# Performance work log

Measured on AMD Instinct MI355X. Metric: run time of the kernel, lower is better.

## Reference

```python
import jax, jax.numpy as jnp
import numpy as np

EPS = 1e-6

def _rotate(z, q):
    # rotation trick (Householder-style reflection chain), z,q: [M, D]
    sg = jax.lax.stop_gradient
    z_norm = z / (jnp.linalg.norm(z, axis=1, keepdims=True) + EPS)
    q_norm = q / (jnp.linalg.norm(q, axis=1, keepdims=True) + EPS)
    w = sg((z_norm + q_norm) / jnp.linalg.norm(z_norm + q_norm, axis=1, keepdims=True))
    zn_d = sg(z_norm)
    qn_d = sg(q_norm)
    e = z - 2.0 * jnp.sum(z * w, axis=1, keepdims=True) * w \
          + 2.0 * jnp.sum(z * zn_d, axis=1, keepdims=True) * qn_d
    scale = sg(jnp.linalg.norm(q, axis=1, keepdims=True) / (jnp.linalg.norm(z, axis=1, keepdims=True) + EPS))
    return e * scale

def setup_inputs() -> dict:
    key = jax.random.key(0)
    k1, k2 = jax.random.split(key)
    x = jax.random.normal(k1, (16, 2048, 512), dtype=jnp.float32)
    codebooks = jax.random.normal(k2, (8, 1024, 512), dtype=jnp.float32)
    return {"x": x, "codebooks": codebooks}

def reference(x, codebooks):
    # x: [B, N, D]; codebooks: [Q, C, D]
    B, N, D = x.shape
    Q, C, _ = codebooks.shape
    sg = jax.lax.stop_gradient
    cb_sq = jnp.sum(codebooks * codebooks, axis=-1)  # [Q, C]
    residual = x
    quantized_out = jnp.zeros_like(x)
    all_indices = []
    all_losses = []
    for qi in range(Q):
        cb = codebooks[qi]                               # [C, D]
        flat = residual.reshape(-1, D)                   # [B*N, D]
        # squared euclidean distance: ||r||^2 - 2 r.c + ||c||^2
        d2 = jnp.sum(flat * flat, axis=1, keepdims=True) - 2.0 * (flat @ cb.T) + cb_sq[qi]
        ind = jnp.argmin(d2, axis=1)                     # [B*N]
        quant_raw = jnp.take(cb, ind, axis=0)            # [B*N, D]
        # commitment loss (codebook frozen per freeze_codebook=True)
        loss = jnp.mean((sg(quant_raw) - flat) ** 2)
        # rotation-trick transform of the quantized vectors
        quant = _rotate(flat, quant_raw).reshape(B, N, D)
        residual = residual - sg(quant)
        quantized_out = quantized_out + quant
        all_indices.append(ind.reshape(B, N))
        all_losses.append(loss)
    all_indices = jnp.stack(all_indices, axis=-1)        # [B, N, Q]
    all_losses = jnp.stack(all_losses, axis=-1)          # [Q]
    return quantized_out, all_indices, all_losses
```

## Files before the change

### kernel.cpp

```cpp
#include <hip/hip_runtime.h>

#define EPS 1e-6f

typedef __attribute__((ext_vector_type(8))) short bf16x8;
typedef __attribute__((ext_vector_type(4))) float f32x4;
typedef __attribute__((ext_vector_type(8))) unsigned short ushort8;

#define AS1(p) ((const __attribute__((address_space(1))) void*)(p))
#define AS3(p) ((__attribute__((address_space(3))) void*)(p))

__device__ inline unsigned int fkey(float f) {
  unsigned int u = __float_as_uint(f);
  return (u & 0x80000000u) ? ~u : (u | 0x80000000u);
}
__device__ inline float inv_fkey(unsigned int k) {
  unsigned int u = (k & 0x80000000u) ? (k & 0x7fffffffu) : ~k;
  return __uint_as_float(u);
}

__device__ inline unsigned long long shfl_xor_u64(unsigned long long v, int mask) {
  unsigned int lo = (unsigned int)(v & 0xffffffffull);
  unsigned int hi = (unsigned int)(v >> 32);
  lo = (unsigned int)__shfl_xor((int)lo, mask);
  hi = (unsigned int)__shfl_xor((int)hi, mask);
  return (((unsigned long long)hi) << 32) | lo;
}

__device__ inline unsigned short f2bf(float f) {
  unsigned int u = __float_as_uint(f);
  u += 0x7fffu + ((u >> 16) & 1u);
  return (unsigned short)(u >> 16);
}
__device__ inline float bf2f(unsigned short h) {
  return __uint_as_float(((unsigned int)h) << 16);
}

__device__ inline unsigned lds_off(const void* p) {
  return (unsigned)(unsigned long long)(__attribute__((address_space(3))) const void*)p;
}

template<int OFF>
__device__ inline bf16x8 ds_read128(unsigned addr) {
  bf16x8 r;
  asm volatile("ds_read_b128 %0, %1 offset:%2" : "=v"(r) : "v"(addr), "i"(OFF));
  return r;
}

template<int OFF>
__device__ inline float gload_f32(unsigned long long a) {
  float r;
  asm volatile("global_load_dword %0, %1, off offset:%2" : "=v"(r) : "v"(a), "i"(OFF));
  return r;
}

__global__ __launch_bounds__(256) void prep_kernel(
    const float* __restrict__ x, const float* __restrict__ cbs,
    unsigned short* __restrict__ Rhi, unsigned short* __restrict__ Rlo,
    unsigned short* __restrict__ CBhi, unsigned short* __restrict__ CBlo,
    float* __restrict__ cbsq, float* __restrict__ loss_out) {
  constexpr size_t M = 32768, D = 512, C = 1024, Q = 8;
  const size_t nthreads = (size_t)gridDim.x * 256;
  const size_t gtid = (size_t)blockIdx.x * 256 + threadIdx.x;
  const int lane = threadIdx.x & 63;
  const int w = threadIdx.x >> 6;

  for (size_t i = gtid; i < M * D / 8; i += nthreads) {
    size_t off = i * 8;
    float4 v0 = *(const float4*)(x + off);
    float4 v1 = *(const float4*)(x + off + 4);
    float v[8] = {v0.x, v0.y, v0.z, v0.w, v1.x, v1.y, v1.z, v1.w};
    ushort8 h, l;
    #pragma unroll
    for (int j = 0; j < 8; j++) {
      unsigned short hh = f2bf(v[j]);
      h[j] = hh;
      l[j] = f2bf(v[j] - bf2f(hh));
    }
    *(ushort8*)(Rhi + off) = h;
    *(ushort8*)(Rlo + off) = l;
  }
  for (size_t i = gtid; i < Q * C * D / 8; i += nthreads) {
    size_t off = i * 8;
    float4 v0 = *(const float4*)(cbs + off);
    float4 v1 = *(const float4*)(cbs + off + 4);
    float v[8] = {v0.x, v0.y, v0.z, v0.w, v1.x, v1.y, v1.z, v1.w};
    ushort8 h, l;
    #pragma unroll
    for (int j = 0; j < 8; j++) {
      unsigned short hh = f2bf(v[j]);
      h[j] = hh;
      l[j] = f2bf(v[j] - bf2f(hh));
    }
    *(ushort8*)(CBhi + off) = h;
    *(ushort8*)(CBlo + off) = l;
  }
  for (int row = blockIdx.x * 4 + w; row < (int)(Q * C); row += gridDim.x * 4) {
    const float4* p = (const float4*)(cbs + (size_t)row * 512);
    float4 v0 = p[lane];
    float4 v1 = p[lane + 64];
    float s = v0.x*v0.x + v0.y*v0.y + v0.z*v0.z + v0.w*v0.w
            + v1.x*v1.x + v1.y*v1.y + v1.z*v1.z + v1.w*v1.w;
    #pragma unroll
    for (int off = 32; off; off >>= 1) s += __shfl_xor(s, off);
    if (lane == 0) cbsq[row] = s;
  }
  if (blockIdx.x == 0 && threadIdx.x < (int)Q) loss_out[threadIdx.x] = 0.f;
}

#define BARRIER  asm volatile("s_barrier" ::: "memory")
#define LGKM0    asm volatile("s_waitcnt lgkmcnt(0)" ::: "memory")
#define SCHEDB   __builtin_amdgcn_sched_barrier(0)

__global__ __launch_bounds__(512, 2) void stage_kernel(
    const float* __restrict__ x, const float* __restrict__ cbs,
    unsigned short* __restrict__ Rhi, unsigned short* __restrict__ Rlo,
    const unsigned short* __restrict__ CBhi, const unsigned short* __restrict__ CBlo,
    const float* __restrict__ cbsq, float* __restrict__ qout,
    float* __restrict__ idx_out, float* __restrict__ loss_out) {
  __shared__ unsigned short As[3][2][128 * 32];
  __shared__ unsigned short Bs[3][2][256 * 32];
  __shared__ unsigned long long bestLDS[4][128];
  __shared__ float ls[8];

  const int tid = threadIdx.x;
  const int lane = tid & 63;
  const int w = tid >> 6;
  const int wr = w >> 2, wc = w & 3;
  const int row0 = blockIdx.x * 128;

  const int rw = lane >> 2, oq = lane & 3;
  const int o_sw = (oq - rw - (rw >> 2)) & 3;
  const int m = lane & 15, g = lane >> 4;
  const int f_sw8 = ((g + m + (m >> 2)) & 3) * 8;

  const unsigned short* pAhi = Rhi + (size_t)(row0 + w * 16 + rw) * 512 + o_sw * 8;
  const unsigned short* pAlo = Rlo + (size_t)(row0 + w * 16 + rw) * 512 + o_sw * 8;

  for (int qi = 0; qi < 8; ++qi) {
    const int last = (qi == 7);
    const size_t cbo = (size_t)qi * 524288;
    const unsigned short* pBhi = CBhi + cbo + (size_t)(w * 32 + rw) * 512 + o_sw * 8;
    const unsigned short* pBlo = CBlo + cbo + (size_t)(w * 32 + rw) * 512 + o_sw * 8;
    const float* cq_base = cbsq + (qi << 10);
    const float* cbq_f32 = cbs + cbo;

    unsigned aA = lds_off(&As[0][0][(wr * 64 + m) * 32 + f_sw8]);
    unsigned aB = lds_off(&Bs[0][0][(wc * 64 + m) * 32 + f_sw8]);

    unsigned long long best[4][4];
    #pragma unroll
    for (int mi = 0; mi < 4; mi++)
      #pragma unroll
      for (int r = 0; r < 4; r++) best[mi][r] = ~0ull;

    auto stageA = [&](int buf, int t) {
      const size_t ko = (size_t)((t & 15) * 32);
      __builtin_amdgcn_global_load_lds(AS1(pAhi + ko), AS3(&As[buf][0][w * 512]), 16, 0, 0);
      __builtin_amdgcn_global_load_lds(AS1(pAlo + ko), AS3(&As[buf][1][w * 512]), 16, 0, 0);
    };
    auto stageB1 = [&](int buf, int t) {
      const size_t ko = (size_t)((t & 15) * 32);
      const size_t cof = (size_t)((t >> 4) * 256) * 512;
      unsigned short* dBh = &Bs[buf][0][w * 1024];
      __builtin_amdgcn_global_load_lds(AS1(pBhi + cof + ko), AS3(dBh), 16, 0, 0);
      __builtin_amdgcn_global_load_lds(AS1(pBhi + cof + ko + 8192), AS3(dBh + 512), 16, 0, 0);
    };
    auto stageB2 = [&](int buf, int t) {
      const size_t ko = (size_t)((t & 15) * 32);
      const size_t cof = (size_t)((t >> 4) * 256) * 512;
      unsigned short* dBl = &Bs[buf][1][w * 1024];
      __builtin_amdgcn_global_load_lds(AS1(pBlo + cof + ko), AS3(dBl), 16, 0, 0);
      __builtin_amdgcn_global_load_lds(AS1(pBlo + cof + ko + 8192), AS3(dBl + 512), 16, 0, 0);
    };

    __syncthreads();

    float cq[4][4];
    {
      unsigned long long cqp = (unsigned long long)(cq_base + wc * 64 + m);
      cq[0][0] = gload_f32<0>(cqp);    cq[0][1] = gload_f32<64>(cqp);
      cq[0][2] = gload_f32<128>(cqp);  cq[0][3] = gload_f32<192>(cqp);
      cq[1][0] = gload_f32<1024>(cqp); cq[1][1] = gload_f32<1088>(cqp);
      cq[1][2] = gload_f32<1152>(cqp); cq[1][3] = gload_f32<1216>(cqp);
      cq[2][0] = gload_f32<2048>(cqp); cq[2][1] = gload_f32<2112>(cqp);
      cq[2][2] = gload_f32<2176>(cqp); cq[2][3] = gload_f32<2240>(cqp);
      cq[3][0] = gload_f32<3072>(cqp); cq[3][1] = gload_f32<3136>(cqp);
      cq[3][2] = gload_f32<3200>(cqp); cq[3][3] = gload_f32<3264>(cqp);
      asm volatile("s_waitcnt vmcnt(0)" ::: "memory");
    }

    stageA(0, 0); stageB1(0, 0); stageB2(0, 0);
    stageA(1, 1); stageB1(1, 1); stageB2(1, 1);
    asm volatile("s_waitcnt vmcnt(6)" ::: "memory");
    BARRIER;
    SCHEDB;

    bf16x8 ah[4], al[4], bh[4], bl[4];
    f32x4 acc[4][4];
    int bn = 0;
    int bst = 2;

    for (int t = 0; t < 64; ++t) {
      const int kk = t & 15;

      ah[0] = ds_read128<0>(aA);     ah[1] = ds_read128<1024>(aA);
      al[0] = ds_read128<8192>(aA);  al[1] = ds_read128<9216>(aA);
      bh[0] = ds_read128<0>(aB);     bh[1] = ds_read128<1024>(aB);
      bl[0] = ds_read128<16384>(aB); bl[1] = ds_read128<17408>(aB);
      if (t < 62) stageA(bst, t + 2);
      if (kk == 0) {
        #pragma unroll
        for (int mi = 0; mi < 4; mi++)
          #pragma unroll
          for (int ni = 0; ni < 4; ni++)
            acc[mi][ni] = (f32x4){0.f, 0.f, 0.f, 0.f};
      }
      BARRIER; LGKM0; SCHEDB;
      __builtin_amdgcn_s_setprio(1);
      #pragma unroll
      for (int mi = 0; mi < 2; mi++)
        #pragma unroll
        for (int ni = 0; ni < 2; ni++)
          acc[mi][ni] = __builtin_amdgcn_mfma_f32_16x16x32_bf16(ah[mi], bh[ni], acc[mi][ni], 0, 0, 0);
      #pragma unroll
      for (int mi = 0; mi < 2; mi++)
        #pragma unroll
        for (int ni = 0; ni < 2; ni++)
          acc[mi][ni] = __builtin_amdgcn_mfma_f32_16x16x32_bf16(ah[mi], bl[ni], acc[mi][ni], 0, 0, 0);
      #pragma unroll
      for (int mi = 0; mi < 2; mi++)
        #pragma unroll
        for (int ni = 0; ni < 2; ni++)
          acc[mi][ni] = __builtin_amdgcn_mfma_f32_16x16x32_bf16(al[mi], bh[ni], acc[mi][ni], 0, 0, 0);
      __builtin_amdgcn_s_setprio(0);
      BARRIER; SCHEDB;

      bh[2] = ds_read128<2048>(aB);  bh[3] = ds_read128<3072>(aB);
      bl[2] = ds_read128<18432>(aB); bl[3] = ds_read128<19456>(aB);
      if (t < 62) stageB1(bst, t + 2);
      BARRIER; LGKM0; SCHEDB;
      __builtin_amdgcn_s_setprio(1);
      #pragma unroll
      for (int mi = 0; mi < 2; mi++)
        #pragma unroll
        for (int ni = 2; ni < 4; ni++)
          acc[mi][ni] = __builtin_amdgcn_mfma_f32_16x16x32_bf16(ah[mi], bh[ni], acc[mi][ni], 0, 0, 0);
      #pragma unroll
      for (int mi = 0; mi < 2; mi++)
        #pragma unroll
        for (int ni = 2; ni < 4; ni++)
          acc[mi][ni] = __builtin_amdgcn_mfma_f32_16x16x32_bf16(ah[mi], bl[ni], acc[mi][ni], 0, 0, 0);
      #pragma unroll
      for (int mi = 0; mi < 2; mi++)
        #pragma unroll
        for (int ni = 2; ni < 4; ni++)
          acc[mi][ni] = __builtin_amdgcn_mfma_f32_16x16x32_bf16(al[mi], bh[ni], acc[mi][ni], 0, 0, 0);
      __builtin_amdgcn_s_setprio(0);
      BARRIER; SCHEDB;

      ah[2] = ds_read128<2048>(aA);  ah[3] = ds_read128<3072>(aA);
      al[2] = ds_read128<10240>(aA); al[3] = ds_read128<11264>(aA);
      if (t < 62) stageB2(bst, t + 2);
      BARRIER; LGKM0; SCHEDB;
      __builtin_amdgcn_s_setprio(1);
      #pragma unroll
      for (int mi = 2; mi < 4; mi++)
        #pragma unroll
        for (int ni = 2; ni < 4; ni++)
          acc[mi][ni] = __builtin_amdgcn_mfma_f32_16x16x32_bf16(ah[mi], bh[ni], acc[mi][ni], 0, 0, 0);
      #pragma unroll
      for (int mi = 2; mi < 4; mi++)
        #pragma unroll
        for (int ni = 2; ni < 4; ni++)
          acc[mi][ni] = __builtin_amdgcn_mfma_f32_16x16x32_bf16(ah[mi], bl[ni], acc[mi][ni], 0, 0, 0);
      #pragma unroll
      for (int mi = 2; mi < 4; mi++)
        #pragma unroll
        for (int ni = 2; ni < 4; ni++)
          acc[mi][ni] = __builtin_amdgcn_mfma_f32_16x16x32_bf16(al[mi], bh[ni], acc[mi][ni], 0, 0, 0);
      __builtin_amdgcn_s_setprio(0);
      BARRIER; SCHEDB;

      __builtin_amdgcn_s_setprio(1);
      #pragma unroll
      for (int mi = 2; mi < 4; mi++)
        #pragma unroll
        for (int ni = 0; ni < 2; ni++)
          acc[mi][ni] = __builtin_amdgcn_mfma_f32_16x16x32_bf16(ah[mi], bh[ni], acc[mi][ni], 0, 0, 0);
      #pragma unroll
      for (int mi = 2; mi < 4; mi++)
        #pragma unroll
        for (int ni = 0; ni < 2; ni++)
          acc[mi][ni] = __builtin_amdgcn_mfma_f32_16x16x32_bf16(ah[mi], bl[ni], acc[mi][ni], 0, 0, 0);
      #pragma unroll
      for (int mi = 2; mi < 4; mi++)
        #pragma unroll
        for (int ni = 0; ni < 2; ni++)
          acc[mi][ni] = __builtin_amdgcn_mfma_f32_16x16x32_bf16(al[mi], bh[ni], acc[mi][ni], 0, 0, 0);
      __builtin_amdgcn_s_setprio(0);
      if (kk == 15) {
        const int ct_ = t >> 4;
        const unsigned colb = ct_ * 256 + wc * 64 + m;
        #pragma unroll
        for (int mi = 0; mi < 4; mi++)
          #pragma unroll
          for (int r = 0; r < 4; r++) {
            #pragma unroll
            for (int ni = 0; ni < 4; ni++) {
              float d2 = fmaf(-2.f, acc[mi][ni][r], cq[ct_][ni]);
              unsigned long long p =
                  (((unsigned long long)fkey(d2)) << 32) | (colb + ni * 16);
              if (p < best[mi][r]) best[mi][r] = p;
            }
          }
      }
      if (t < 62) asm volatile("s_waitcnt vmcnt(6)" ::: "memory");
      else        asm volatile("s_waitcnt vmcnt(0)" ::: "memory");
      BARRIER; SCHEDB;

      const int s_ = (bn == 2) ? -2 : 1;
      aA += s_ * 16384; aB += s_ * 32768;
      bn = (bn == 2) ? 0 : bn + 1;
      bst = (bst == 2) ? 0 : bst + 1;
    }

    #pragma unroll
    for (int mi = 0; mi < 4; mi++)
      #pragma unroll
      for (int r = 0; r < 4; r++) {
        unsigned long long mn = best[mi][r];
        #pragma unroll
        for (int off = 1; off < 16; off <<= 1) {
          unsigned long long o = shfl_xor_u64(mn, off);
          if (o < mn) mn = o;
        }
        best[mi][r] = mn;
      }

    if (m == 0) {
      #pragma unroll
      for (int mi = 0; mi < 4; mi++)
        #pragma unroll
        for (int r = 0; r < 4; r++)
          bestLDS[wc][wr * 64 + mi * 16 + g * 4 + r] = best[mi][r];
    }
    __syncthreads();

    float lossacc = 0.f;
    #pragma unroll 2
    for (int rr = 0; rr < 16; rr++) {
      const int row128 = w * 16 + rr;
      unsigned long long mn = bestLDS[0][row128];
      #pragma unroll
      for (int q2 = 1; q2 < 4; q2++) {
        unsigned long long o = bestLDS[q2][row128];
        if (o < mn) mn = o;
      }
      const int c = (int)(mn & 0xffffffffu);
      const int row = row0 + row128;
      if (lane == 0) idx_out[(size_t)row * 8 + qi] = (float)c;

      const float qq = cq_base[c];
      const float d2b = inv_fkey((unsigned)(mn >> 32));
      const float zq = (qq - d2b) * 0.5f;

      const size_t base = (size_t)row * 512 + lane * 8;
      ushort8 h = *(const ushort8*)(Rhi + base);
      ushort8 l = *(const ushort8*)(Rlo + base);
      const float* qrow = cbq_f32 + (size_t)c * 512 + lane * 8;
      float4 q0 = *(const float4*)qrow;
      float4 q1 = *(const float4*)(qrow + 4);
      float z[8], q[8] = {q0.x, q0.y, q0.z, q0.w, q1.x, q1.y, q1.z, q1.w};
      #pragma unroll
      for (int j = 0; j < 8; j++) z[j] = bf2f(h[j]) + bf2f(l[j]);

      float zz = 0.f;
      #pragma unroll
      for (int j = 0; j < 8; j++) zz = fmaf(z[j], z[j], zz);
      #pragma unroll
      for (int off = 32; off; off >>= 1) zz += __shfl_xor(zz, off);

      float nz = sqrtf(zz), nq = sqrtf(qq);
      float inz = 1.f / (nz + EPS), inq = 1.f / (nq + EPS);
      float ns  = sqrtf(zz*inz*inz + 2.f*zq*inz*inq + qq*inq*inq);
      float ins = 1.f / ns;
      float zw  = (zz*inz + zq*inq) * ins;
      float zzn = zz * inz;
      float scale = nq * inz;
      float az = scale * (1.f - 2.f * zw * ins * inz);
      float aq = scale * (2.f * zzn - 2.f * zw * ins) * inq;

      if (!last) {
        #pragma unroll
        for (int j = 0; j < 8; j++) {
          float r = z[j] - (az * z[j] + aq * q[j]);
          unsigned short hh = f2bf(r);
          h[j] = hh;
          l[j] = f2bf(r - bf2f(hh));
        }
        *(ushort8*)(Rhi + base) = h;
        *(ushort8*)(Rlo + base) = l;
      } else {
        float4 x0 = *(const float4*)(x + base);
        float4 x1 = *(const float4*)(x + base + 4);
        float xv[8] = {x0.x, x0.y, x0.z, x0.w, x1.x, x1.y, x1.z, x1.w};
        float o[8];
        #pragma unroll
        for (int j = 0; j < 8; j++) {
          float r = z[j] - (az * z[j] + aq * q[j]);
          o[j] = xv[j] - r;
        }
        *(float4*)(qout + base)     = (float4){o[0], o[1], o[2], o[3]};
        *(float4*)(qout + base + 4) = (float4){o[4], o[5], o[6], o[7]};
      }
      lossacc += (zz - 2.f * zq + qq);
    }
    if (lane == 0) ls[w] = lossacc;
    __syncthreads();
    if (tid == 0)
      atomicAdd(loss_out + qi, (ls[0] + ls[1] + ls[2] + ls[3] +
                                ls[4] + ls[5] + ls[6] + ls[7]) *
                               (1.f / (32768.f * 512.f)));
  }
}

extern "C" void kernel_launch(void* const* d_in, const int* in_sizes, int n_in,
                              void* d_out, int out_size, void* d_ws, size_t ws_size,
                              hipStream_t stream) {
  const float* x   = (const float*)d_in[0];
  const float* cbs = (const float*)d_in[1];
  float* out = (float*)d_out;
  const size_t M = 32768, D = 512, Q = 8, C = 1024;
  float* qout     = out;
  float* idx_out  = out + M * D;
  float* loss_out = idx_out + M * Q;

  unsigned short* Rhi  = (unsigned short*)d_ws;
  unsigned short* Rlo  = Rhi + M * D;
  unsigned short* CBhi = Rlo + M * D;
  unsigned short* CBlo = CBhi + Q * C * D;
  float* cbsq = (float*)(CBlo + Q * C * D);

  prep_kernel<<<512, 256, 0, stream>>>(x, cbs, Rhi, Rlo, CBhi, CBlo, cbsq, loss_out);

  stage_kernel<<<256, 512, 0, stream>>>(
      x, cbs, Rhi, Rlo, CBhi, CBlo, cbsq, qout, idx_out, loss_out);
}
```

Baseline: 1.089 ms.

## Software-pipeline LDS fragment reads across K iterations with register double buffering

Restructures the bf16-split GEMM main loop so the A/B fragments for the next K step are read from LDS during the current step's MFMA phases, using double-buffered register arrays and a two-step unrolled loop. Full lgkmcnt(0) waits become partial lgkmcnt(4) waits, and the global vmcnt wait moves earlier into the second phase, so LDS latency overlaps with MFMA work. This raises register pressure (extra fragment buffers) under launch_bounds(512,2) and makes barrier and wait-count correctness more delicate.

```diff
diff --git a/kernel.cpp b/kernel.cpp
--- a/kernel.cpp
+++ b/kernel.cpp
@@ -108,8 +108,10 @@
 }
 
 #define BARRIER  asm volatile("s_barrier" ::: "memory")
-#define LGKM0    asm volatile("s_waitcnt lgkmcnt(0)" ::: "memory")
 #define SCHEDB   __builtin_amdgcn_sched_barrier(0)
+#define LGKM(N)  asm volatile("s_waitcnt lgkmcnt(" #N ")" ::: "memory")
+#define VMC(N)   asm volatile("s_waitcnt vmcnt(" #N ")" ::: "memory")
+#define MFMA1(d, a, b) d = __builtin_amdgcn_mfma_f32_16x16x32_bf16(a, b, d, 0, 0, 0)
 
 __global__ __launch_bounds__(512, 2) void stage_kernel(
     const float* __restrict__ x, const float* __restrict__ cbs,
@@ -186,143 +188,132 @@
       cq[2][2] = gload_f32<2176>(cqp); cq[2][3] = gload_f32<2240>(cqp);
       cq[3][0] = gload_f32<3072>(cqp); cq[3][1] = gload_f32<3136>(cqp);
       cq[3][2] = gload_f32<3200>(cqp); cq[3][3] = gload_f32<3264>(cqp);
-      asm volatile("s_waitcnt vmcnt(0)" ::: "memory");
-    }
-
-    stageA(0, 0); stageB1(0, 0); stageB2(0, 0);
-    stageA(1, 1); stageB1(1, 1); stageB2(1, 1);
-    asm volatile("s_waitcnt vmcnt(6)" ::: "memory");
-    BARRIER;
-    SCHEDB;
-
-    bf16x8 ah[4], al[4], bh[4], bl[4];
+      VMC(0);
+    }
+
+    bf16x8 A01h[2][2], A01l[2][2], B01h[2][2], B01l[2][2];
+    bf16x8 A23h[2], A23l[2], B23h[2], B23l[2];
     f32x4 acc[4][4];
     int bn = 0;
     int bst = 2;
 
-    for (int t = 0; t < 64; ++t) {
-      const int kk = t & 15;
-
-      ah[0] = ds_read128<0>(aA);     ah[1] = ds_read128<1024>(aA);
-      al[0] = ds_read128<8192>(aA);  al[1] = ds_read128<9216>(aA);
-      bh[0] = ds_read128<0>(aB);     bh[1] = ds_read128<1024>(aB);
-      bl[0] = ds_read128<16384>(aB); bl[1] = ds_read128<17408>(aB);
-      if (t < 62) stageA(bst, t + 2);
-      if (kk == 0) {
-        #pragma unroll
-        for (int mi = 0; mi < 4; mi++)
-          #pragma unroll
-          for (int ni = 0; ni < 4; ni++)
-            acc[mi][ni] = (f32x4){0.f, 0.f, 0.f, 0.f};
-      }
-      BARRIER; LGKM0; SCHEDB;
-      __builtin_amdgcn_s_setprio(1);
-      #pragma unroll
-      for (int mi = 0; mi < 2; mi++)
-        #pragma unroll
-        for (int ni = 0; ni < 2; ni++)
-          acc[mi][ni] = __builtin_amdgcn_mfma_f32_16x16x32_bf16(ah[mi], bh[ni], acc[mi][ni], 0, 0, 0);
-      #pragma unroll
-      for (int mi = 0; mi < 2; mi++)
-        #pragma unroll
-        for (int ni = 0; ni < 2; ni++)
-          acc[mi][ni] = __builtin_amdgcn_mfma_f32_16x16x32_bf16(ah[mi], bl[ni], acc[mi][ni], 0, 0, 0);
-      #pragma unroll
-      for (int mi = 0; mi < 2; mi++)
-        #pragma unroll
-        for (int ni = 0; ni < 2; ni++)
-          acc[mi][ni] = __builtin_amdgcn_mfma_f32_16x16x32_bf16(al[mi], bh[ni], acc[mi][ni], 0, 0, 0);
-      __builtin_amdgcn_s_setprio(0);
-      BARRIER; SCHEDB;
-
-      bh[2] = ds_read128<2048>(aB);  bh[3] = ds_read128<3072>(aB);
-      bl[2] = ds_read128<18432>(aB); bl[3] = ds_read128<19456>(aB);
-      if (t < 62) stageB1(bst, t + 2);
-      BARRIER; LGKM0; SCHEDB;
-      __builtin_amdgcn_s_setprio(1);
-      #pragma unroll
-      for (int mi = 0; mi < 2; mi++)
-        #pragma unroll
-        for (int ni = 2; ni < 4; ni++)
-          acc[mi][ni] = __builtin_amdgcn_mfma_f32_16x16x32_bf16(ah[mi], bh[ni], acc[mi][ni], 0, 0, 0);
-      #pragma unroll
-      for (int mi = 0; mi < 2; mi++)
-        #pragma unroll
-        for (int ni = 2; ni < 4; ni++)
-          acc[mi][ni] = __builtin_amdgcn_mfma_f32_16x16x32_bf16(ah[mi], bl[ni], acc[mi][ni], 0, 0, 0);
-      #pragma unroll
-      for (int mi = 0; mi < 2; mi++)
-        #pragma unroll
-        for (int ni = 2; ni < 4; ni++)
-          acc[mi][ni] = __builtin_amdgcn_mfma_f32_16x16x32_bf16(al[mi], bh[ni], acc[mi][ni], 0, 0, 0);
-      __builtin_amdgcn_s_setprio(0);
-      BARRIER; SCHEDB;
-
-      ah[2] = ds_read128<2048>(aA);  ah[3] = ds_read128<3072>(aA);
-      al[2] = ds_read128<10240>(aA); al[3] = ds_read128<11264>(aA);
-      if (t < 62) stageB2(bst, t + 2);
-      BARRIER; LGKM0; SCHEDB;
-      __builtin_amdgcn_s_setprio(1);
-      #pragma unroll
-      for (int mi = 2; mi < 4; mi++)
-        #pragma unroll
-        for (int ni = 2; ni < 4; ni++)
-          acc[mi][ni] = __builtin_amdgcn_mfma_f32_16x16x32_bf16(ah[mi], bh[ni], acc[mi][ni], 0, 0, 0);
-      #pragma unroll
-      for (int mi = 2; mi < 4; mi++)
-        #pragma unroll
-        for (int ni = 2; ni < 4; ni++)
-          acc[mi][ni] = __builtin_amdgcn_mfma_f32_16x16x32_bf16(ah[mi], bl[ni], acc[mi][ni], 0, 0, 0);
-      #pragma unroll
-      for (int mi = 2; mi < 4; mi++)
-        #pragma unroll
-        for (int ni = 2; ni < 4; ni++)
-          acc[mi][ni] = __builtin_amdgcn_mfma_f32_16x16x32_bf16(al[mi], bh[ni], acc[mi][ni], 0, 0, 0);
-      __builtin_amdgcn_s_setprio(0);
-      BARRIER; SCHEDB;
-
-      __builtin_amdgcn_s_setprio(1);
-      #pragma unroll
-      for (int mi = 2; mi < 4; mi++)
-        #pragma unroll
-        for (int ni = 0; ni < 2; ni++)
-          acc[mi][ni] = __builtin_amdgcn_mfma_f32_16x16x32_bf16(ah[mi], bh[ni], acc[mi][ni], 0, 0, 0);
-      #pragma unroll
-      for (int mi = 2; mi < 4; mi++)
-        #pragma unroll
-        for (int ni = 0; ni < 2; ni++)
-          acc[mi][ni] = __builtin_amdgcn_mfma_f32_16x16x32_bf16(ah[mi], bl[ni], acc[mi][ni], 0, 0, 0);
-      #pragma unroll
-      for (int mi = 2; mi < 4; mi++)
-        #pragma unroll
-        for (int ni = 0; ni < 2; ni++)
-          acc[mi][ni] = __builtin_amdgcn_mfma_f32_16x16x32_bf16(al[mi], bh[ni], acc[mi][ni], 0, 0, 0);
-      __builtin_amdgcn_s_setprio(0);
-      if (kk == 15) {
-        const int ct_ = t >> 4;
-        const unsigned colb = ct_ * 256 + wc * 64 + m;
-        #pragma unroll
-        for (int mi = 0; mi < 4; mi++)
-          #pragma unroll
-          for (int r = 0; r < 4; r++) {
-            #pragma unroll
-            for (int ni = 0; ni < 4; ni++) {
-              float d2 = fmaf(-2.f, acc[mi][ni][r], cq[ct_][ni]);
-              unsigned long long p =
-                  (((unsigned long long)fkey(d2)) << 32) | (colb + ni * 16);
-              if (p < best[mi][r]) best[mi][r] = p;
-            }
-          }
-      }
-      if (t < 62) asm volatile("s_waitcnt vmcnt(6)" ::: "memory");
-      else        asm volatile("s_waitcnt vmcnt(0)" ::: "memory");
-      BARRIER; SCHEDB;
-
-      const int s_ = (bn == 2) ? -2 : 1;
-      aA += s_ * 16384; aB += s_ * 32768;
-      bn = (bn == 2) ? 0 : bn + 1;
-      bst = (bst == 2) ? 0 : bst + 1;
-    }
+    stageA(0, 0); stageB1(0, 0); stageB2(0, 0);
+    stageA(1, 1); stageB1(1, 1); stageB2(1, 1);
+    VMC(6);
+    BARRIER; SCHEDB;
+    A01h[0][0] = ds_read128<0>(aA);     A01h[0][1] = ds_read128<1024>(aA);
+    A01l[0][0] = ds_read128<8192>(aA);  A01l[0][1] = ds_read128<9216>(aA);
+    B01h[0][0] = ds_read128<0>(aB);     B01h[0][1] = ds_read128<1024>(aB);
+    B01l[0][0] = ds_read128<16384>(aB); B01l[0][1] = ds_read128<17408>(aB);
+    LGKM(4);
+    SCHEDB;
+
+#define K_ITER(T, CS, RD)                                                         \
+  {                                                                               \
+    const int t_ = (T);                                                           \
+    const int kk_ = t_ & 15;                                                      \
+    const int s_ = (bn == 2) ? -2 : 1;                                            \
+    const unsigned aA2 = aA + s_ * 16384, aB2 = aB + s_ * 32768;                  \
+             \
+    B23h[0] = ds_read128<2048>(aB);  B23h[1] = ds_read128<3072>(aB);              \
+    B23l[0] = ds_read128<18432>(aB); B23l[1] = ds_read128<19456>(aB);             \
+    if (t_ < 62) stageA(bst, t_ + 2);                                             \
+    if (kk_ == 0) {                                                               \
+      _Pragma("unroll") for (int mi = 0; mi < 4; mi++)                            \
+        _Pragma("unroll") for (int ni = 0; ni < 4; ni++)                          \
+          acc[mi][ni] = (f32x4){0.f, 0.f, 0.f, 0.f};                              \
+    }                                                                             \
+    BARRIER; LGKM(4); SCHEDB;                                                     \
+    __builtin_amdgcn_s_setprio(1);                                                \
+    _Pragma("unroll") for (int i = 0; i < 2; i++)                                 \
+      _Pragma("unroll") for (int j = 0; j < 2; j++)                               \
+        MFMA1(acc[i][j], A01h[CS][i], B01h[CS][j]);                               \
+    _Pragma("unroll") for (int i = 0; i < 2; i++)                                 \
+      _Pragma("unroll") for (int j = 0; j < 2; j++)                               \
+        MFMA1(acc[i][j], A01h[CS][i], B01l[CS][j]);                               \
+    _Pragma("unroll") for (int i = 0; i < 2; i++)                                 \
+      _Pragma("unroll") for (int j = 0; j < 2; j++)                               \
+        MFMA1(acc[i][j], A01l[CS][i], B01h[CS][j]);                               \
+    __builtin_amdgcn_s_setprio(0);                                                \
+       \
+    A23h[0] = ds_read128<2048>(aA);  A23h[1] = ds_read128<3072>(aA);              \
+    A23l[0] = ds_read128<10240>(aA); A23l[1] = ds_read128<11264>(aA);             \
+    if (t_ < 62) { stageB1(bst, t_ + 2); VMC(4); }                                \
+    else if (t_ == 62) VMC(0);                                                    \
+    BARRIER; LGKM(4); SCHEDB;                                                     \
+    __builtin_amdgcn_s_setprio(1);                                                \
+    _Pragma("unroll") for (int i = 0; i < 2; i++)                                 \
+      _Pragma("unroll") for (int j = 0; j < 2; j++)                               \
+        MFMA1(acc[i][2 + j], A01h[CS][i], B23h[j]);                               \
+    _Pragma("unroll") for (int i = 0; i < 2; i++)                                 \
+      _Pragma("unroll") for (int j = 0; j < 2; j++)                               \
+        MFMA1(acc[i][2 + j], A01h[CS][i], B23l[j]);                               \
+    _Pragma("unroll") for (int i = 0; i < 2; i++)                                 \
+      _Pragma("unroll") for (int j = 0; j < 2; j++)                               \
+        MFMA1(acc[i][2 + j], A01l[CS][i], B23h[j]);                               \
+    __builtin_amdgcn_s_setprio(0);                                                \
+             \
+    if (t_ < 63) {                                                                \
+      A01h[RD][0] = ds_read128<0>(aA2);    A01h[RD][1] = ds_read128<1024>(aA2);   \
+      A01l[RD][0] = ds_read128<8192>(aA2); A01l[RD][1] = ds_read128<9216>(aA2);   \
+    }                                                                             \
+    if (t_ < 62) stageB2(bst, t_ + 2);                                            \
+    BARRIER;                                                                      \
+    if (t_ < 63) { LGKM(4); } else { LGKM(0); }                                   \
+    SCHEDB;                                                                       \
+    __builtin_amdgcn_s_setprio(1);                                                \
+    _Pragma("unroll") for (int i = 0; i < 2; i++)                                 \
+      _Pragma("unroll") for (int j = 0; j < 2; j++)                               \
+        MFMA1(acc[2 + i][2 + j], A23h[i], B23h[j]);                               \
+    _Pragma("unroll") for (int i = 0; i < 2; i++)                                 \
+      _Pragma("unroll") for (int j = 0; j < 2; j++)                               \
+        MFMA1(acc[2 + i][2 + j], A23h[i], B23l[j]);                               \
+    _Pragma("unroll") for (int i = 0; i < 2; i++)                                 \
+      _Pragma("unroll") for (int j = 0; j < 2; j++)                               \
+        MFMA1(acc[2 + i][2 + j], A23l[i], B23h[j]);                               \
+    __builtin_amdgcn_s_setprio(0);                                                \
+                 \
+    if (t_ < 63) {                                                                \
+      B01h[RD][0] = ds_read128<0>(aB2);     B01h[RD][1] = ds_read128<1024>(aB2);  \
+      B01l[RD][0] = ds_read128<16384>(aB2); B01l[RD][1] = ds_read128<17408>(aB2); \
+    }                                                                             \
+    BARRIER;                                                                      \
+    if (t_ < 63) { LGKM(4); } else { LGKM(0); }                                   \
+    SCHEDB;                                                                       \
+    __builtin_amdgcn_s_setprio(1);                                                \
+    _Pragma("unroll") for (int i = 0; i < 2; i++)                                 \
+      _Pragma("unroll") for (int j = 0; j < 2; j++)                               \
+        MFMA1(acc[2 + i][j], A23h[i], B01h[CS][j]);                               \
+    _Pragma("unroll") for (int i = 0; i < 2; i++)                                 \
+      _Pragma("unroll") for (int j = 0; j < 2; j++)                               \
+        MFMA1(acc[2 + i][j], A23h[i], B01l[CS][j]);                               \
+    _Pragma("unroll") for (int i = 0; i < 2; i++)                                 \
+      _Pragma("unroll") for (int j = 0; j < 2; j++)                               \
+        MFMA1(acc[2 + i][j], A23l[i], B01h[CS][j]);                               \
+    __builtin_amdgcn_s_setprio(0);                                                \
+    if (kk_ == 15) {                                                              \
+      const int ct_ = t_ >> 4;                                                    \
+      const unsigned colb = ct_ * 256 + wc * 64 + m;                              \
+      _Pragma("unroll") for (int mi = 0; mi < 4; mi++)                            \
+        _Pragma("unroll") for (int r = 0; r < 4; r++) {                           \
+          _Pragma("unroll") for (int ni = 0; ni < 4; ni++) {                      \
+            float d2 = fmaf(-2.f, acc[mi][ni][r], cq[ct_][ni]);                   \
+            unsigned long long p =                                                \
+                (((unsigned long long)fkey(d2)) << 32) | (colb + ni * 16);        \
+            if (p < best[mi][r]) best[mi][r] = p;                                 \
+          }                                                                       \
+        }                                                                         \
+    }                                                                             \
+    aA = aA2; aB = aB2;                                                           \
+    bn = (bn == 2) ? 0 : bn + 1;                                                  \
+    bst = (bst == 2) ? 0 : bst + 1;                                               \
+  }
+
+    for (int tp = 0; tp < 32; tp++) {
+      K_ITER(tp * 2,     0, 1);
+      K_ITER(tp * 2 + 1, 1, 0);
+    }
+#undef K_ITER
 
     #pragma unroll
     for (int mi = 0; mi < 4; mi++)
```

Measured after the change: 981.9 us. 1.11x faster.
